# Kernel tuning notes

Measured on AMD Instinct MI355X. Metric: run time of the kernel, lower is better.

Reference implementation:

```python
import jax, jax.numpy as jnp
import numpy as np

N_NODES = 100000
N_EDGES = 1600000
IN_DIM = 128
OUT_DIM = 128
NEG_SLOPE = 0.2


def setup_inputs() -> dict:
    key = jax.random.key(0)
    ks = jax.random.split(key, 7)
    x = jax.random.normal(ks[0], (N_NODES, IN_DIM), dtype=jnp.float32)
    edge_index = jax.random.randint(ks[1], (2, N_EDGES), 0, N_NODES, dtype=jnp.int32)
    # xavier-ish scale for [in, out] weight layout (y = x @ W)
    s = float(np.sqrt(2.0 / (IN_DIM + OUT_DIM)))
    W_q = jax.random.normal(ks[2], (IN_DIM, OUT_DIM), dtype=jnp.float32) * s
    W_k = jax.random.normal(ks[3], (IN_DIM, OUT_DIM), dtype=jnp.float32) * s
    W_v = jax.random.normal(ks[4], (IN_DIM, OUT_DIM), dtype=jnp.float32) * s
    W_l = jax.random.normal(ks[5], (IN_DIM, OUT_DIM), dtype=jnp.float32) * s
    b_l = jnp.zeros((OUT_DIM,), dtype=jnp.float32)
    return {"x": x, "edge_index": edge_index, "W_q": W_q, "W_k": W_k,
            "W_v": W_v, "W_l": W_l, "b_l": b_l}


def reference(x, edge_index, W_q, W_k, W_v, W_l, b_l):
    num_nodes = x.shape[0]
    row, col = edge_index[0], edge_index[1]

    h_q = x @ W_q                                   # [N, D]
    h_k = x @ W_k                                   # [N, D]
    _h_v = x @ W_v                                  # computed in original, unused downstream

    # aggregated query: sum of neighbor queries per destination node
    q_agg = jax.ops.segment_sum(h_q[col], row, num_segments=num_nodes)  # [N, D]
    k_act = jax.nn.leaky_relu(h_k, NEG_SLOPE)

    # per-edge attention scores (note: original uses raw q_agg, not activated)
    scores = jnp.sum(k_act[row] * q_agg[col], axis=1) / (OUT_DIM ** 0.5)  # [E]

    # scatter-softmax over edges grouped by destination (row)
    max_val = jax.ops.segment_max(scores, row, num_segments=num_nodes)
    exp_scores = jnp.exp(scores - max_val[row])
    sum_exp = jax.ops.segment_sum(exp_scores, row, num_segments=num_nodes)
    alpha = exp_scores / (sum_exp[row] + 1e-8)      # [E]; dropout is identity in eval

    h_proj = x @ W_l + b_l                          # [N, D]
    weighted = alpha[:, None] * h_proj[col]         # [E, D]
    h_prime = jax.ops.segment_sum(weighted, row, num_segments=num_nodes)
    return jax.nn.leaky_relu(h_prime, NEG_SLOPE)
```

## Files before the change

kernel.cpp:

```cpp
#include <hip/hip_runtime.h>
#include <math.h>

#define N_NODES 100000
#define N_EDGES 1600000
#define DIM 128
#define CAP 64

#define NB1 196
#define NPB 512
#define CHUNK1 4096
#define GRID1 391
#define SLOT1 52
#define LSTRIDE 197

typedef short bf16x8 __attribute__((ext_vector_type(8)));
typedef float f32x4 __attribute__((ext_vector_type(4)));

static __device__ __forceinline__ unsigned bf16rne(float f) {
    unsigned u = __float_as_uint(f);
    return (u + 0x7FFFu + ((u >> 16) & 1u)) >> 16;
}
static __device__ __forceinline__ float bflo(unsigned u) { return __uint_as_float(u << 16); }
static __device__ __forceinline__ float bfhi(unsigned u) { return __uint_as_float(u & 0xFFFF0000u); }


__global__ __launch_bounds__(256) void pb_k(
    const float* __restrict__ x, const float* __restrict__ Wq,
    const float* __restrict__ Wk, const float* __restrict__ Wl,
    const int* __restrict__ row, const int* __restrict__ col,
    ushort* __restrict__ xb, ushort* __restrict__ kactb,
    ushort* __restrict__ WqTh, ushort* __restrict__ WqTl,
    ushort* __restrict__ WlTh, ushort* __restrict__ WlTl,
    unsigned* __restrict__ bkt, int* __restrict__ bktc) {
    __shared__ uint4 smem4[4352];
    int j = blockIdx.x, t = threadIdx.x;

    if (j % 3 == 2) {
        int blk = j / 3;
        int* lcnt = (int*)smem4;
        unsigned* lbuf = (unsigned*)smem4 + 256;
        if (t < NB1) lcnt[t] = 0;
        __syncthreads();
        long base = (long)blk * CHUNK1;
        if (base + CHUNK1 <= N_EDGES) {
            const uint4* r4 = (const uint4*)row + (size_t)blk * 1024;
            const uint4* c4 = (const uint4*)col + (size_t)blk * 1024;
#pragma unroll
            for (int q = 0; q < 4; q++) {
                uint4 rv = r4[q * 256 + t];
                uint4 cv = c4[q * 256 + t];
                unsigned rr[4] = {rv.x, rv.y, rv.z, rv.w};
                unsigned cc[4] = {cv.x, cv.y, cv.z, cv.w};
#pragma unroll
                for (int i = 0; i < 4; i++) {
                    int b = rr[i] >> 9;
                    int p = atomicAdd(&lcnt[b], 1);
                    if (p < SLOT1) lbuf[p * LSTRIDE + b] = (cc[i] << 9) | (rr[i] & 511u);
                }
            }
        } else {
            for (int i = t; base + i < N_EDGES; i += 256) {
                unsigned r = (unsigned)row[base + i], c = (unsigned)col[base + i];
                int b = r >> 9;
                int p = atomicAdd(&lcnt[b], 1);
                if (p < SLOT1) lbuf[p * LSTRIDE + b] = (c << 9) | (r & 511u);
            }
        }
        __syncthreads();
        if (t < NB1) bktc[(size_t)blk * NB1 + t] = min(lcnt[t], SLOT1);
        int wave = t >> 6, lane = t & 63;
        for (int s = wave; s < NB1; s += 4) {
            if (lane < min(lcnt[s], SLOT1))
                bkt[((size_t)s * GRID1 + blk) * SLOT1 + lane] = lbuf[lane * LSTRIDE + s];
        }
        return;
    }

    int p = (j / 3) * 2 + (j % 3);
    ushort* bh = (ushort*)smem4;
    ushort* blo = (ushort*)smem4 + 128 * 136;

    if (p < 2) {
        const float* W = (p == 0) ? Wq : Wl;
        ushort* Th = (p == 0) ? WqTh : WlTh;
        ushort* Tl = (p == 0) ? WqTl : WlTl;
        for (int i = t; i < 16384; i += 256) {
            int k = i >> 7, n = i & 127;
            float v = W[i];
            unsigned hi = bf16rne(v);
            float lo = v - bflo(hi);
            Th[n * 128 + k] = (ushort)hi;
            Tl[n * 128 + k] = (ushort)bf16rne(lo);
        }
    }
    for (int i = t; i < 16384; i += 256) {
        int k = i >> 7, n = i & 127;
        float v = Wk[i];
        unsigned hi = bf16rne(v);
        float lo = v - bflo(hi);
        bh[n * 136 + k] = (ushort)hi;
        blo[n * 136 + k] = (ushort)bf16rne(lo);
    }
    __syncthreads();

    int wave = t >> 6, lane = t & 63;
    int ln15 = lane & 15, quad = lane >> 4;
    long base = (long)p * 128 + wave * 32;

    bf16x8 Af[2][4];
#pragma unroll
    for (int r = 0; r < 2; r++) {
        long rw = base + r * 16 + ln15;
        long rowc = rw < N_NODES ? rw : N_NODES - 1;
#pragma unroll
        for (int s = 0; s < 4; s++) {
            int ch = s * 4 + quad;
            const float4* xp = (const float4*)(x + rowc * 128 + ch * 8);
            float4 u0 = xp[0], u1 = xp[1];
            bf16x8 f;
            f[0] = (short)bf16rne(u0.x); f[1] = (short)bf16rne(u0.y);
            f[2] = (short)bf16rne(u0.z); f[3] = (short)bf16rne(u0.w);
            f[4] = (short)bf16rne(u1.x); f[5] = (short)bf16rne(u1.y);
            f[6] = (short)bf16rne(u1.z); f[7] = (short)bf16rne(u1.w);
            Af[r][s] = f;
            if (rw < N_NODES) *(bf16x8*)(xb + rw * 128 + ch * 8) = f;
        }
    }
    f32x4 acc[2][8];
#pragma unroll
    for (int r = 0; r < 2; r++)
#pragma unroll
        for (int t8 = 0; t8 < 8; t8++) acc[r][t8] = (f32x4){0.f, 0.f, 0.f, 0.f};
#pragma unroll
    for (int phase = 0; phase < 2; phase++) {
        const ushort* B = phase ? blo : bh;
#pragma unroll
        for (int s = 0; s < 4; s++) {
#pragma unroll
            for (int t8 = 0; t8 < 8; t8++) {
                bf16x8 b = *(const bf16x8*)(B + (t8 * 16 + ln15) * 136 + (s * 4 + quad) * 8);
                acc[0][t8] = __builtin_amdgcn_mfma_f32_16x16x32_bf16(Af[0][s], b, acc[0][t8], 0, 0, 0);
                acc[1][t8] = __builtin_amdgcn_mfma_f32_16x16x32_bf16(Af[1][s], b, acc[1][t8], 0, 0, 0);
            }
        }
    }
#pragma unroll
    for (int r = 0; r < 2; r++) {
#pragma unroll
        for (int reg = 0; reg < 4; reg++) {
            long node = base + r * 16 + quad * 4 + reg;
            if (node < N_NODES) {
#pragma unroll
                for (int t8 = 0; t8 < 8; t8++) {
                    float v = acc[r][t8][reg];
                    v = v > 0.f ? v : 0.2f * v;
                    kactb[node * 128 + t8 * 16 + ln15] = (ushort)bf16rne(v);
                }
            }
        }
    }
}


__global__ __launch_bounds__(1024) void build_k(const int* __restrict__ bktc,
                                                const unsigned* __restrict__ bkt,
                                                int* __restrict__ cur,
                                                int* __restrict__ scol) {
    __shared__ int lcur[NPB];
    __shared__ int lc[GRID1];
    int b = blockIdx.x, t = threadIdx.x;
    if (t < NPB) lcur[t] = 0;
    if (t < GRID1) lc[t] = bktc[(size_t)t * NB1 + b];
    __syncthreads();
    int wave = t >> 6, lane = t & 63;
    const unsigned* D = bkt + (size_t)b * GRID1 * SLOT1;
    for (int s = wave; s < GRID1; s += 16) {
        if (lane < lc[s]) {
            unsigned v = D[(size_t)s * SLOT1 + lane];
            int rl = (int)(v & 511u);
            int c = (int)(v >> 9);
            int p = atomicAdd(&lcur[rl], 1);
            if (p < CAP) scol[((size_t)b * NPB + rl) * CAP + p] = c;
        }
    }
    __syncthreads();
    if (t < NPB) {
        int node = b * NPB + t;
        if (node < N_NODES) cur[node] = lcur[t];
    }
}


__global__ __launch_bounds__(256) void xq_k(const uint4* __restrict__ xb4,
                                            const int* __restrict__ cur,
                                            const int* __restrict__ scol,
                                            const ushort* __restrict__ BTh,
                                            const ushort* __restrict__ BTl,
                                            uint4* __restrict__ qx4) {
    __shared__ ushort lxa[16][136];
    __shared__ ushort lq[16][136];
    int t = threadIdx.x;
    int g16 = t >> 4, gl = t & 15;
    long node = (long)blockIdx.x * 16 + g16;
    int d = min(cur[node], CAP);
    float a0 = 0.f, a1 = 0.f, a2 = 0.f, a3 = 0.f;
    float a4 = 0.f, a5 = 0.f, a6 = 0.f, a7 = 0.f;
    for (int j = 0; j < d; j += 16) {
        int cb = (j + gl < d) ? scol[node * CAP + j + gl] : 0;
        int lim = min(16, d - j);
        int k = 0;
        for (; k + 4 <= lim; k += 4) {
            int c0 = __shfl(cb, k, 16),     c1 = __shfl(cb, k + 1, 16);
            int c2 = __shfl(cb, k + 2, 16), c3 = __shfl(cb, k + 3, 16);
            uint4 u0 = xb4[(size_t)c0 * 16 + gl];
            uint4 u1 = xb4[(size_t)c1 * 16 + gl];
            uint4 u2 = xb4[(size_t)c2 * 16 + gl];
            uint4 u3 = xb4[(size_t)c3 * 16 + gl];
            a0 += bflo(u0.x); a1 += bfhi(u0.x); a2 += bflo(u0.y); a3 += bfhi(u0.y);
            a4 += bflo(u0.z); a5 += bfhi(u0.z); a6 += bflo(u0.w); a7 += bfhi(u0.w);
            a0 += bflo(u1.x); a1 += bfhi(u1.x); a2 += bflo(u1.y); a3 += bfhi(u1.y);
            a4 += bflo(u1.z); a5 += bfhi(u1.z); a6 += bflo(u1.w); a7 += bfhi(u1.w);
            a0 += bflo(u2.x); a1 += bfhi(u2.x); a2 += bflo(u2.y); a3 += bfhi(u2.y);
            a4 += bflo(u2.z); a5 += bfhi(u2.z); a6 += bflo(u2.w); a7 += bfhi(u2.w);
            a0 += bflo(u3.x); a1 += bfhi(u3.x); a2 += bflo(u3.y); a3 += bfhi(u3.y);
            a4 += bflo(u3.z); a5 += bfhi(u3.z); a6 += bflo(u3.w); a7 += bfhi(u3.w);
        }
        for (; k < lim; k++) {
            int c = __shfl(cb, k, 16);
            uint4 u = xb4[(size_t)c * 16 + gl];
            a0 += bflo(u.x); a1 += bfhi(u.x); a2 += bflo(u.y); a3 += bfhi(u.y);
            a4 += bflo(u.z); a5 += bfhi(u.z); a6 += bflo(u.w); a7 += bfhi(u.w);
        }
    }
    uint4 o;
    o.x = bf16rne(a0) | (bf16rne(a1) << 16);
    o.y = bf16rne(a2) | (bf16rne(a3) << 16);
    o.z = bf16rne(a4) | (bf16rne(a5) << 16);
    o.w = bf16rne(a6) | (bf16rne(a7) << 16);
    *(uint4*)&lxa[g16][gl * 8] = o;
    __syncthreads();

    int wave = t >> 6, lane = t & 63;
    int ln15 = lane & 15, quad = (lane >> 4) & 3;
    const bf16x8* Bh8 = (const bf16x8*)BTh;
    const bf16x8* Bl8 = (const bf16x8*)BTl;
    bf16x8 af[4];
#pragma unroll
    for (int s = 0; s < 4; s++)
        af[s] = *(const bf16x8*)&lxa[ln15][(s * 4 + quad) * 8];
#pragma unroll
    for (int ti = 0; ti < 2; ti++) {
        int ct = wave * 2 + ti;
        f32x4 acc = (f32x4){0.f, 0.f, 0.f, 0.f};
#pragma unroll
        for (int phase = 0; phase < 2; phase++) {
            const bf16x8* B8 = phase ? Bl8 : Bh8;
#pragma unroll
            for (int s = 0; s < 4; s++)
                acc = __builtin_amdgcn_mfma_f32_16x16x32_bf16(
                    af[s], B8[(ct * 16 + ln15) * 16 + s * 4 + quad], acc, 0, 0, 0);
        }
#pragma unroll
        for (int reg = 0; reg < 4; reg++)
            lq[quad * 4 + reg][ct * 16 + ln15] = (ushort)bf16rne(acc[reg]);
    }
    __syncthreads();

    const uint2* xb2 = (const uint2*)xb4;
#pragma unroll
    for (int i = 0; i < 2; i++) {
        int idx = i * 256 + t;
        int g = idx >> 5, c = idx & 31;
        long n2 = (long)blockIdx.x * 16 + g;
        uint2 q2 = *(const uint2*)&lq[g][c * 4];
        uint2 x2 = xb2[n2 * 32 + c];
        qx4[n2 * 32 + c] = make_uint4(q2.x, q2.y, x2.x, x2.y);
    }
}


__global__ __launch_bounds__(256) void attn_k(const uint2* __restrict__ kactb,
                                              const uint4* __restrict__ qx4,
                                              const int* __restrict__ cur,
                                              const int* __restrict__ scol,
                                              uint2* __restrict__ xwb,
                                              float* __restrict__ sumw) {
    int g = (blockIdx.x * 256 + threadIdx.x) >> 5;
    int lane = threadIdx.x & 31;
    int d = min(cur[g], CAP);
    uint2 ku = kactb[(size_t)g * 32 + lane];
    const float scale = 0.08838834764831845f;
    float k0 = bflo(ku.x) * scale, k1 = bfhi(ku.x) * scale;
    float k2 = bflo(ku.y) * scale, k3 = bfhi(ku.y) * scale;

    float S = 0.f;
    float a0 = 0.f, a1 = 0.f, a2 = 0.f, a3 = 0.f;
    for (int j = 0; j < d; j += 32) {
        int cb = (j + lane < d) ? scol[g * CAP + j + lane] : 0;
        int lim = min(32, d - j);
        int k = 0;
        for (; k + 4 <= lim; k += 4) {
            int c0 = __shfl(cb, k, 32),     c1 = __shfl(cb, k + 1, 32);
            int c2 = __shfl(cb, k + 2, 32), c3 = __shfl(cb, k + 3, 32);
            uint4 u0 = qx4[(size_t)c0 * 32 + lane];
            uint4 u1 = qx4[(size_t)c1 * 32 + lane];
            uint4 u2 = qx4[(size_t)c2 * 32 + lane];
            uint4 u3 = qx4[(size_t)c3 * 32 + lane];
            float p0 = k0 * bflo(u0.x) + k1 * bfhi(u0.x) + k2 * bflo(u0.y) + k3 * bfhi(u0.y);
            float p1 = k0 * bflo(u1.x) + k1 * bfhi(u1.x) + k2 * bflo(u1.y) + k3 * bfhi(u1.y);
            float p2 = k0 * bflo(u2.x) + k1 * bfhi(u2.x) + k2 * bflo(u2.y) + k3 * bfhi(u2.y);
            float p3 = k0 * bflo(u3.x) + k1 * bfhi(u3.x) + k2 * bflo(u3.y) + k3 * bfhi(u3.y);
#pragma unroll
            for (int off = 16; off > 0; off >>= 1) {
                p0 += __shfl_xor(p0, off, 32); p1 += __shfl_xor(p1, off, 32);
                p2 += __shfl_xor(p2, off, 32); p3 += __shfl_xor(p3, off, 32);
            }
            float e0 = __expf(p0), e1 = __expf(p1);
            float e2 = __expf(p2), e3 = __expf(p3);
            S += (e0 + e1) + (e2 + e3);
            a0 += e0 * bflo(u0.z) + e1 * bflo(u1.z) + e2 * bflo(u2.z) + e3 * bflo(u3.z);
            a1 += e0 * bfhi(u0.z) + e1 * bfhi(u1.z) + e2 * bfhi(u2.z) + e3 * bfhi(u3.z);
            a2 += e0 * bflo(u0.w) + e1 * bflo(u1.w) + e2 * bflo(u2.w) + e3 * bflo(u3.w);
            a3 += e0 * bfhi(u0.w) + e1 * bfhi(u1.w) + e2 * bfhi(u2.w) + e3 * bfhi(u3.w);
        }
        for (; k < lim; k++) {
            int c = __shfl(cb, k, 32);
            uint4 u = qx4[(size_t)c * 32 + lane];
            float p = k0 * bflo(u.x) + k1 * bfhi(u.x) + k2 * bflo(u.y) + k3 * bfhi(u.y);
#pragma unroll
            for (int off = 16; off > 0; off >>= 1) p += __shfl_xor(p, off, 32);
            float e0 = __expf(p);
            S += e0;
            a0 += e0 * bflo(u.z);
            a1 += e0 * bfhi(u.z);
            a2 += e0 * bflo(u.w);
            a3 += e0 * bfhi(u.w);
        }
    }
    float inv = 1.f / (S + 1e-8f);
    uint2 o;
    o.x = bf16rne(a0 * inv) | (bf16rne(a1 * inv) << 16);
    o.y = bf16rne(a2 * inv) | (bf16rne(a3 * inv) << 16);
    xwb[(size_t)g * 32 + lane] = o;
    if (lane == 0) sumw[g] = S * inv;
}


__global__ __launch_bounds__(256) void fin_k(const ushort* __restrict__ Ab,
                                             const ushort* __restrict__ BTh,
                                             const ushort* __restrict__ BTl,
                                             const float* __restrict__ bl,
                                             const float* __restrict__ sumw,
                                             float* __restrict__ out) {
    int tid = threadIdx.x;
    int wave = tid >> 6, lane = tid & 63;
    int ln15 = lane & 15, quad = (lane >> 4) & 3;
    long base = (long)blockIdx.x * 128 + wave * 32;

    const bf16x8* A8 = (const bf16x8*)Ab;
    const bf16x8* Bh8 = (const bf16x8*)BTh;
    const bf16x8* Bl8 = (const bf16x8*)BTl;

    bf16x8 Af[2][4];
#pragma unroll
    for (int r = 0; r < 2; r++) {
        long row = base + r * 16 + ln15;
#pragma unroll
        for (int s = 0; s < 4; s++) Af[r][s] = A8[row * 16 + s * 4 + quad];
    }
    float blv[8];
#pragma unroll
    for (int t = 0; t < 8; t++) blv[t] = bl[t * 16 + ln15];

    f32x4 acc[2][8];
#pragma unroll
    for (int r = 0; r < 2; r++)
#pragma unroll
        for (int t = 0; t < 8; t++) acc[r][t] = (f32x4){0.f, 0.f, 0.f, 0.f};

#pragma unroll
    for (int phase = 0; phase < 2; phase++) {
        const bf16x8* B8 = phase ? Bl8 : Bh8;
#pragma unroll
        for (int s = 0; s < 4; s++) {
#pragma unroll
            for (int t = 0; t < 8; t++) {
                bf16x8 b = B8[(t * 16 + ln15) * 16 + s * 4 + quad];
                acc[0][t] = __builtin_amdgcn_mfma_f32_16x16x32_bf16(Af[0][s], b, acc[0][t], 0, 0, 0);
                acc[1][t] = __builtin_amdgcn_mfma_f32_16x16x32_bf16(Af[1][s], b, acc[1][t], 0, 0, 0);
            }
        }
    }
#pragma unroll
    for (int r = 0; r < 2; r++) {
#pragma unroll
        for (int reg = 0; reg < 4; reg++) {
            long node = base + r * 16 + quad * 4 + reg;
            if (node < N_NODES) {
                float sw = sumw[node];
#pragma unroll
                for (int t = 0; t < 8; t++) {
                    float v = acc[r][t][reg] + sw * blv[t];
                    v = v > 0.f ? v : 0.2f * v;
                    out[node * 128 + t * 16 + ln15] = v;
                }
            }
        }
    }
}


extern "C" void kernel_launch(void* const* d_in, const int* in_sizes, int n_in,
                              void* d_out, int out_size, void* d_ws, size_t ws_size,
                              hipStream_t stream) {
    const float* x  = (const float*)d_in[0];
    const int* row  = (const int*)d_in[1];
    const int* col  = row + N_EDGES;
    const float* Wq = (const float*)d_in[2];
    const float* Wk = (const float*)d_in[3];
    const float* Wl = (const float*)d_in[5];
    const float* bl = (const float*)d_in[6];
    float* out = (float*)d_out;

    ushort* xb    = (ushort*)d_ws;
    ushort* qx    = xb + (size_t)N_NODES * DIM;
    ushort* kactb = qx + (size_t)N_NODES * 256;
    ushort* xwb   = kactb + (size_t)N_NODES * DIM;
    ushort* wbuf  = xwb + (size_t)N_NODES * DIM;
    ushort* WqTh = wbuf,             *WqTl = wbuf + 16384;
    ushort* WlTh = wbuf + 2 * 16384, *WlTl = wbuf + 3 * 16384;
    float* sumw = (float*)(wbuf + 4 * 16384);
    int* cur  = (int*)(sumw + N_NODES);
    int* scol = cur + N_NODES;
    unsigned* bkt = (unsigned*)(scol + (size_t)N_NODES * CAP);
    int* bktc = (int*)(bkt + (size_t)NB1 * GRID1 * SLOT1);

    pb_k<<<1173, 256, 0, stream>>>(x, Wq, Wk, Wl, row, col, xb, kactb,
                                   WqTh, WqTl, WlTh, WlTl, bkt, bktc);
    build_k<<<NB1, 1024, 0, stream>>>(bktc, bkt, cur, scol);
    xq_k<<<N_NODES / 16, 256, 0, stream>>>((const uint4*)xb, cur, scol,
                                           WqTh, WqTl, (uint4*)qx);
    attn_k<<<N_NODES / 8, 256, 0, stream>>>((const uint2*)kactb, (const uint4*)qx,
                                            cur, scol, (uint2*)xwb, sumw);
    fin_k<<<(N_NODES + 127) / 128, 256, 0, stream>>>(xwb, WlTh, WlTl, bl, sumw, out);
}
```

Baseline: 458.5 us.

## Split neighbor gathers across a full wave per node and halve pb_k LDS

The neighbor-sum stage in xq_k now gives each node a whole 64-lane wave: four 16-lane groups handle different edges and are combined with cross-lane shuffles. attn_k now uses one 64-lane wave per node instead of a half-wave, with the two halves taking alternating edges and being reduced at the end; its grid doubles to match. pb_k now holds one bf16 copy of Wk in LDS, computing with the high part and then refilling the same buffer with the low part, so shared memory per block drops by about 40%. The aim is more parallel gathers per node and higher occupancy, at the cost of extra shuffles, an extra barrier, and more idle lanes on low-degree nodes.

```diff
diff --git a/kernel.cpp b/kernel.cpp
--- a/kernel.cpp
+++ b/kernel.cpp
@@ -32,7 +32,7 @@
     ushort* __restrict__ WqTh, ushort* __restrict__ WqTl,
     ushort* __restrict__ WlTh, ushort* __restrict__ WlTl,
     unsigned* __restrict__ bkt, int* __restrict__ bktc) {
-    __shared__ uint4 smem4[4352];
+    __shared__ uint4 smem4[2625];
     int j = blockIdx.x, t = threadIdx.x;
 
     if (j % 3 == 2) {
@@ -77,8 +77,7 @@
     }
 
     int p = (j / 3) * 2 + (j % 3);
-    ushort* bh = (ushort*)smem4;
-    ushort* blo = (ushort*)smem4 + 128 * 136;
+    ushort* bw = (ushort*)smem4;
 
     if (p < 2) {
         const float* W = (p == 0) ? Wq : Wl;
@@ -95,13 +94,8 @@
     }
     for (int i = t; i < 16384; i += 256) {
         int k = i >> 7, n = i & 127;
-        float v = Wk[i];
-        unsigned hi = bf16rne(v);
-        float lo = v - bflo(hi);
-        bh[n * 136 + k] = (ushort)hi;
-        blo[n * 136 + k] = (ushort)bf16rne(lo);
-    }
-    __syncthreads();
+        bw[n * 136 + k] = (ushort)bf16rne(Wk[i]);
+    }
 
     int wave = t >> 6, lane = t & 63;
     int ln15 = lane & 15, quad = lane >> 4;
@@ -131,17 +125,33 @@
     for (int r = 0; r < 2; r++)
 #pragma unroll
         for (int t8 = 0; t8 < 8; t8++) acc[r][t8] = (f32x4){0.f, 0.f, 0.f, 0.f};
-#pragma unroll
-    for (int phase = 0; phase < 2; phase++) {
-        const ushort* B = phase ? blo : bh;
-#pragma unroll
-        for (int s = 0; s < 4; s++) {
-#pragma unroll
-            for (int t8 = 0; t8 < 8; t8++) {
-                bf16x8 b = *(const bf16x8*)(B + (t8 * 16 + ln15) * 136 + (s * 4 + quad) * 8);
-                acc[0][t8] = __builtin_amdgcn_mfma_f32_16x16x32_bf16(Af[0][s], b, acc[0][t8], 0, 0, 0);
-                acc[1][t8] = __builtin_amdgcn_mfma_f32_16x16x32_bf16(Af[1][s], b, acc[1][t8], 0, 0, 0);
-            }
+
+    __syncthreads();
+#pragma unroll
+    for (int s = 0; s < 4; s++) {
+#pragma unroll
+        for (int t8 = 0; t8 < 8; t8++) {
+            bf16x8 b = *(const bf16x8*)(bw + (t8 * 16 + ln15) * 136 + (s * 4 + quad) * 8);
+            acc[0][t8] = __builtin_amdgcn_mfma_f32_16x16x32_bf16(Af[0][s], b, acc[0][t8], 0, 0, 0);
+            acc[1][t8] = __builtin_amdgcn_mfma_f32_16x16x32_bf16(Af[1][s], b, acc[1][t8], 0, 0, 0);
+        }
+    }
+    __syncthreads();
+    for (int i = t; i < 16384; i += 256) {
+        int k = i >> 7, n = i & 127;
+        float v = Wk[i];
+        unsigned hi = bf16rne(v);
+        float lo = v - bflo(hi);
+        bw[n * 136 + k] = (ushort)bf16rne(lo);
+    }
+    __syncthreads();
+#pragma unroll
+    for (int s = 0; s < 4; s++) {
+#pragma unroll
+        for (int t8 = 0; t8 < 8; t8++) {
+            bf16x8 b = *(const bf16x8*)(bw + (t8 * 16 + ln15) * 136 + (s * 4 + quad) * 8);
+            acc[0][t8] = __builtin_amdgcn_mfma_f32_16x16x32_bf16(Af[0][s], b, acc[0][t8], 0, 0, 0);
+            acc[1][t8] = __builtin_amdgcn_mfma_f32_16x16x32_bf16(Af[1][s], b, acc[1][t8], 0, 0, 0);
         }
     }
 #pragma unroll
@@ -200,47 +210,57 @@
     __shared__ ushort lxa[16][136];
     __shared__ ushort lq[16][136];
     int t = threadIdx.x;
-    int g16 = t >> 4, gl = t & 15;
-    long node = (long)blockIdx.x * 16 + g16;
-    int d = min(cur[node], CAP);
-    float a0 = 0.f, a1 = 0.f, a2 = 0.f, a3 = 0.f;
-    float a4 = 0.f, a5 = 0.f, a6 = 0.f, a7 = 0.f;
-    for (int j = 0; j < d; j += 16) {
-        int cb = (j + gl < d) ? scol[node * CAP + j + gl] : 0;
-        int lim = min(16, d - j);
+    int wave = t >> 6, lane = t & 63;
+    int e = lane >> 4;
+    int gl = lane & 15;
+    long blkbase = (long)blockIdx.x * 16;
+
+#pragma unroll
+    for (int i = 0; i < 4; i++) {
+        int li = wave * 4 + i;
+        long node = blkbase + li;
+        int d = min(cur[node], CAP);
+        int cb = (lane < d) ? scol[node * CAP + lane] : 0;
+        float a0 = 0.f, a1 = 0.f, a2 = 0.f, a3 = 0.f;
+        float a4 = 0.f, a5 = 0.f, a6 = 0.f, a7 = 0.f;
         int k = 0;
-        for (; k + 4 <= lim; k += 4) {
-            int c0 = __shfl(cb, k, 16),     c1 = __shfl(cb, k + 1, 16);
-            int c2 = __shfl(cb, k + 2, 16), c3 = __shfl(cb, k + 3, 16);
+        for (; k + 8 <= d; k += 8) {
+            int c0 = __shfl(cb, k + e, 64);
+            int c1 = __shfl(cb, k + 4 + e, 64);
             uint4 u0 = xb4[(size_t)c0 * 16 + gl];
             uint4 u1 = xb4[(size_t)c1 * 16 + gl];
-            uint4 u2 = xb4[(size_t)c2 * 16 + gl];
-            uint4 u3 = xb4[(size_t)c3 * 16 + gl];
             a0 += bflo(u0.x); a1 += bfhi(u0.x); a2 += bflo(u0.y); a3 += bfhi(u0.y);
             a4 += bflo(u0.z); a5 += bfhi(u0.z); a6 += bflo(u0.w); a7 += bfhi(u0.w);
             a0 += bflo(u1.x); a1 += bfhi(u1.x); a2 += bflo(u1.y); a3 += bfhi(u1.y);
             a4 += bflo(u1.z); a5 += bfhi(u1.z); a6 += bflo(u1.w); a7 += bfhi(u1.w);
-            a0 += bflo(u2.x); a1 += bfhi(u2.x); a2 += bflo(u2.y); a3 += bfhi(u2.y);
-            a4 += bflo(u2.z); a5 += bfhi(u2.z); a6 += bflo(u2.w); a7 += bfhi(u2.w);
-            a0 += bflo(u3.x); a1 += bfhi(u3.x); a2 += bflo(u3.y); a3 += bfhi(u3.y);
-            a4 += bflo(u3.z); a5 += bfhi(u3.z); a6 += bflo(u3.w); a7 += bfhi(u3.w);
-        }
-        for (; k < lim; k++) {
-            int c = __shfl(cb, k, 16);
+        }
+        for (; k < d; k += 4) {
+            int c = __shfl(cb, k + e, 64);
             uint4 u = xb4[(size_t)c * 16 + gl];
-            a0 += bflo(u.x); a1 += bfhi(u.x); a2 += bflo(u.y); a3 += bfhi(u.y);
-            a4 += bflo(u.z); a5 += bfhi(u.z); a6 += bflo(u.w); a7 += bfhi(u.w);
-        }
-    }
-    uint4 o;
-    o.x = bf16rne(a0) | (bf16rne(a1) << 16);
-    o.y = bf16rne(a2) | (bf16rne(a3) << 16);
-    o.z = bf16rne(a4) | (bf16rne(a5) << 16);
-    o.w = bf16rne(a6) | (bf16rne(a7) << 16);
-    *(uint4*)&lxa[g16][gl * 8] = o;
-    __syncthreads();
-
-    int wave = t >> 6, lane = t & 63;
+            if (k + e < d) {
+                a0 += bflo(u.x); a1 += bfhi(u.x); a2 += bflo(u.y); a3 += bfhi(u.y);
+                a4 += bflo(u.z); a5 += bfhi(u.z); a6 += bflo(u.w); a7 += bfhi(u.w);
+            }
+        }
+        a0 += __shfl_xor(a0, 16, 64); a1 += __shfl_xor(a1, 16, 64);
+        a2 += __shfl_xor(a2, 16, 64); a3 += __shfl_xor(a3, 16, 64);
+        a4 += __shfl_xor(a4, 16, 64); a5 += __shfl_xor(a5, 16, 64);
+        a6 += __shfl_xor(a6, 16, 64); a7 += __shfl_xor(a7, 16, 64);
+        a0 += __shfl_xor(a0, 32, 64); a1 += __shfl_xor(a1, 32, 64);
+        a2 += __shfl_xor(a2, 32, 64); a3 += __shfl_xor(a3, 32, 64);
+        a4 += __shfl_xor(a4, 32, 64); a5 += __shfl_xor(a5, 32, 64);
+        a6 += __shfl_xor(a6, 32, 64); a7 += __shfl_xor(a7, 32, 64);
+        if (e == 0) {
+            uint4 o;
+            o.x = bf16rne(a0) | (bf16rne(a1) << 16);
+            o.y = bf16rne(a2) | (bf16rne(a3) << 16);
+            o.z = bf16rne(a4) | (bf16rne(a5) << 16);
+            o.w = bf16rne(a6) | (bf16rne(a7) << 16);
+            *(uint4*)&lxa[li][gl * 8] = o;
+        }
+    }
+    __syncthreads();
+
     int ln15 = lane & 15, quad = (lane >> 4) & 3;
     const bf16x8* Bh8 = (const bf16x8*)BTh;
     const bf16x8* Bl8 = (const bf16x8*)BTl;
@@ -271,7 +291,7 @@
     for (int i = 0; i < 2; i++) {
         int idx = i * 256 + t;
         int g = idx >> 5, c = idx & 31;
-        long n2 = (long)blockIdx.x * 16 + g;
+        long n2 = blkbase + g;
         uint2 q2 = *(const uint2*)&lq[g][c * 4];
         uint2 x2 = xb2[n2 * 32 + c];
         qx4[n2 * 32 + c] = make_uint4(q2.x, q2.y, x2.x, x2.y);
@@ -285,51 +305,67 @@
                                               const int* __restrict__ scol,
                                               uint2* __restrict__ xwb,
                                               float* __restrict__ sumw) {
-    int g = (blockIdx.x * 256 + threadIdx.x) >> 5;
-    int lane = threadIdx.x & 31;
+    long g = (blockIdx.x * 256 + threadIdx.x) >> 6;
+    int lane = threadIdx.x & 63;
+    int l31 = lane & 31;
+    int h = lane >> 5;
     int d = min(cur[g], CAP);
-    uint2 ku = kactb[(size_t)g * 32 + lane];
+    uint2 ku = kactb[(size_t)g * 32 + l31];
     const float scale = 0.08838834764831845f;
     float k0 = bflo(ku.x) * scale, k1 = bfhi(ku.x) * scale;
     float k2 = bflo(ku.y) * scale, k3 = bfhi(ku.y) * scale;
 
+    int cb = (lane < d) ? scol[g * CAP + lane] : 0;
     float S = 0.f;
     float a0 = 0.f, a1 = 0.f, a2 = 0.f, a3 = 0.f;
-    for (int j = 0; j < d; j += 32) {
-        int cb = (j + lane < d) ? scol[g * CAP + j + lane] : 0;
-        int lim = min(32, d - j);
-        int k = 0;
-        for (; k + 4 <= lim; k += 4) {
-            int c0 = __shfl(cb, k, 32),     c1 = __shfl(cb, k + 1, 32);
-            int c2 = __shfl(cb, k + 2, 32), c3 = __shfl(cb, k + 3, 32);
-            uint4 u0 = qx4[(size_t)c0 * 32 + lane];
-            uint4 u1 = qx4[(size_t)c1 * 32 + lane];
-            uint4 u2 = qx4[(size_t)c2 * 32 + lane];
-            uint4 u3 = qx4[(size_t)c3 * 32 + lane];
-            float p0 = k0 * bflo(u0.x) + k1 * bfhi(u0.x) + k2 * bflo(u0.y) + k3 * bfhi(u0.y);
-            float p1 = k0 * bflo(u1.x) + k1 * bfhi(u1.x) + k2 * bflo(u1.y) + k3 * bfhi(u1.y);
-            float p2 = k0 * bflo(u2.x) + k1 * bfhi(u2.x) + k2 * bflo(u2.y) + k3 * bfhi(u2.y);
-            float p3 = k0 * bflo(u3.x) + k1 * bfhi(u3.x) + k2 * bflo(u3.y) + k3 * bfhi(u3.y);
-#pragma unroll
-            for (int off = 16; off > 0; off >>= 1) {
-                p0 += __shfl_xor(p0, off, 32); p1 += __shfl_xor(p1, off, 32);
-                p2 += __shfl_xor(p2, off, 32); p3 += __shfl_xor(p3, off, 32);
-            }
-            float e0 = __expf(p0), e1 = __expf(p1);
-            float e2 = __expf(p2), e3 = __expf(p3);
-            S += (e0 + e1) + (e2 + e3);
-            a0 += e0 * bflo(u0.z) + e1 * bflo(u1.z) + e2 * bflo(u2.z) + e3 * bflo(u3.z);
-            a1 += e0 * bfhi(u0.z) + e1 * bfhi(u1.z) + e2 * bfhi(u2.z) + e3 * bfhi(u3.z);
-            a2 += e0 * bflo(u0.w) + e1 * bflo(u1.w) + e2 * bflo(u2.w) + e3 * bflo(u3.w);
-            a3 += e0 * bfhi(u0.w) + e1 * bfhi(u1.w) + e2 * bfhi(u2.w) + e3 * bfhi(u3.w);
-        }
-        for (; k < lim; k++) {
-            int c = __shfl(cb, k, 32);
-            uint4 u = qx4[(size_t)c * 32 + lane];
-            float p = k0 * bflo(u.x) + k1 * bfhi(u.x) + k2 * bflo(u.y) + k3 * bfhi(u.y);
-#pragma unroll
-            for (int off = 16; off > 0; off >>= 1) p += __shfl_xor(p, off, 32);
-            float e0 = __expf(p);
+    int k = 0;
+    for (; k + 8 <= d; k += 8) {
+        int c0 = __shfl(cb, k + h, 64);
+        int c1 = __shfl(cb, k + 2 + h, 64);
+        int c2 = __shfl(cb, k + 4 + h, 64);
+        int c3 = __shfl(cb, k + 6 + h, 64);
+        uint4 u0 = qx4[(size_t)c0 * 32 + l31];
+        uint4 u1 = qx4[(size_t)c1 * 32 + l31];
+        uint4 u2 = qx4[(size_t)c2 * 32 + l31];
+        uint4 u3 = qx4[(size_t)c3 * 32 + l31];
+        float p0 = k0 * bflo(u0.x) + k1 * bfhi(u0.x) + k2 * bflo(u0.y) + k3 * bfhi(u0.y);
+        float p1 = k0 * bflo(u1.x) + k1 * bfhi(u1.x) + k2 * bflo(u1.y) + k3 * bfhi(u1.y);
+        float p2 = k0 * bflo(u2.x) + k1 * bfhi(u2.x) + k2 * bflo(u2.y) + k3 * bfhi(u2.y);
+        float p3 = k0 * bflo(u3.x) + k1 * bfhi(u3.x) + k2 * bflo(u3.y) + k3 * bfhi(u3.y);
+#pragma unroll
+        for (int off = 16; off > 0; off >>= 1) {
+            p0 += __shfl_xor(p0, off, 32); p1 += __shfl_xor(p1, off, 32);
+            p2 += __shfl_xor(p2, off, 32); p3 += __shfl_xor(p3, off, 32);
+        }
+        float e0 = __expf(p0), e1 = __expf(p1);
+        float e2 = __expf(p2), e3 = __expf(p3);
+        S += (e0 + e1) + (e2 + e3);
+        a0 += e0 * bflo(u0.z) + e1 * bflo(u1.z) + e2 * bflo(u2.z) + e3 * bflo(u3.z);
+        a1 += e0 * bfhi(u0.z) + e1 * bfhi(u1.z) + e2 * bfhi(u2.z) + e3 * bfhi(u3.z);
+        a2 += e0 * bflo(u0.w) + e1 * bflo(u1.w) + e2 * bflo(u2.w) + e3 * bflo(u3.w);
+        a3 += e0 * bfhi(u0.w) + e1 * bfhi(u1.w) + e2 * bfhi(u2.w) + e3 * bfhi(u3.w);
+    }
+    for (; k + 2 <= d; k += 2) {
+        int c = __shfl(cb, k + h, 64);
+        uint4 u = qx4[(size_t)c * 32 + l31];
+        float p = k0 * bflo(u.x) + k1 * bfhi(u.x) + k2 * bflo(u.y) + k3 * bfhi(u.y);
+#pragma unroll
+        for (int off = 16; off > 0; off >>= 1) p += __shfl_xor(p, off, 32);
+        float e0 = __expf(p);
+        S += e0;
+        a0 += e0 * bflo(u.z);
+        a1 += e0 * bfhi(u.z);
+        a2 += e0 * bflo(u.w);
+        a3 += e0 * bfhi(u.w);
+    }
+    if (k < d) {
+        int c = __shfl(cb, k, 64);
+        uint4 u = qx4[(size_t)c * 32 + l31];
+        float p = k0 * bflo(u.x) + k1 * bfhi(u.x) + k2 * bflo(u.y) + k3 * bfhi(u.y);
+#pragma unroll
+        for (int off = 16; off > 0; off >>= 1) p += __shfl_xor(p, off, 32);
+        float e0 = __expf(p);
+        if (h == 0) {
             S += e0;
             a0 += e0 * bflo(u.z);
             a1 += e0 * bfhi(u.z);
@@ -337,12 +373,19 @@
             a3 += e0 * bfhi(u.w);
         }
     }
+    S += __shfl_xor(S, 32, 64);
+    a0 += __shfl_xor(a0, 32, 64);
+    a1 += __shfl_xor(a1, 32, 64);
+    a2 += __shfl_xor(a2, 32, 64);
+    a3 += __shfl_xor(a3, 32, 64);
     float inv = 1.f / (S + 1e-8f);
-    uint2 o;
-    o.x = bf16rne(a0 * inv) | (bf16rne(a1 * inv) << 16);
-    o.y = bf16rne(a2 * inv) | (bf16rne(a3 * inv) << 16);
-    xwb[(size_t)g * 32 + lane] = o;
-    if (lane == 0) sumw[g] = S * inv;
+    if (h == 0) {
+        uint2 o;
+        o.x = bf16rne(a0 * inv) | (bf16rne(a1 * inv) << 16);
+        o.y = bf16rne(a2 * inv) | (bf16rne(a3 * inv) << 16);
+        xwb[(size_t)g * 32 + l31] = o;
+        if (l31 == 0) sumw[g] = S * inv;
+    }
 }
 
 
@@ -440,7 +483,7 @@
     build_k<<<NB1, 1024, 0, stream>>>(bktc, bkt, cur, scol);
     xq_k<<<N_NODES / 16, 256, 0, stream>>>((const uint4*)xb, cur, scol,
                                            WqTh, WqTl, (uint4*)qx);
-    attn_k<<<N_NODES / 8, 256, 0, stream>>>((const uint2*)kactb, (const uint4*)qx,
+    attn_k<<<N_NODES / 4, 256, 0, stream>>>((const uint2*)kactb, (const uint4*)qx,
                                             cur, scol, (uint2*)xwb, sumw);
     fin_k<<<(N_NODES + 127) / 128, 256, 0, stream>>>(xwb, WlTh, WlTl, bl, sumw, out);
 }
```

Measured after the change: 462.3 us. Within noise of the previous version (+0.8%).
